# Optimization experiments

Hardware: AMD Instinct MI355X
Metric: run time of the kernel (lower is better)

Reference implementation:

```python
import jax, jax.numpy as jnp
import numpy as np


def normalize_adj(adj):
    """Symmetrize (adj + adj.T*(adj.T>adj) - adj*(adj.T>adj)), add self loops, row-normalize D^-1 A."""
    at = jnp.swapaxes(adj, -1, -2)
    mask = (at > adj).astype(adj.dtype)
    a = adj + at * mask - adj * mask
    m = a.shape[-1]
    a = a + jnp.eye(m, dtype=a.dtype)
    rowsum = a.sum(axis=-1, keepdims=True)
    inv = jnp.where(rowsum > 0, 1.0 / rowsum, 0.0)
    return a * inv


def setup_inputs() -> dict:
    key = jax.random.key(0)
    ks = jax.random.split(key, 8)
    N, n, T, dim, M = 4, 3, 512, 2048, 256
    x = jax.random.normal(ks[0], (N, n, T, dim), dtype=jnp.float32)
    nodes = jax.random.normal(ks[1], (N, M, dim), dtype=jnp.float32)
    adj = (jax.random.uniform(ks[2], (N, M, M)) < 0.05).astype(jnp.float32)
    conv_w = jax.random.normal(ks[3], (2048, dim, 3), dtype=jnp.float32) * 0.02  # OIH
    conv_b = jnp.zeros((2048,), dtype=jnp.float32)
    W1 = jax.random.normal(ks[4], (dim, dim), dtype=jnp.float32) * 0.02
    b1 = jnp.zeros((dim,), dtype=jnp.float32)
    W2 = jax.random.normal(ks[5], (dim, dim), dtype=jnp.float32) * 0.02
    b2 = jnp.zeros((dim,), dtype=jnp.float32)
    return {"x": x, "nodes": nodes, "adj": adj, "conv_w": conv_w, "conv_b": conv_b,
            "W1": W1, "b1": b1, "W2": W2, "b2": b2}


def reference(x, nodes, adj, conv_w, conv_b, W1, b1, W2, b2):
    N, n, T, dim = x.shape
    # Conv1d front-end: (N*n, C=dim, T), kernel 3, pad 1, then ReLU
    feats = x.reshape(N * n, T, dim).transpose(0, 2, 1)  # [B, C, T]
    feats = jax.lax.conv_general_dilated(
        feats, conv_w, window_strides=(1,), padding=[(1, 1)],
        dimension_numbers=("NCH", "OIH", "NCH"))
    feats = jax.nn.relu(feats + conv_b[None, :, None])
    feats = feats.transpose(0, 2, 1).reshape(N, n, T, dim)
    # GCN_Module over per-sample node graphs (batched over N)
    a = normalize_adj(adj)                                   # [N, M, M]
    h = jax.nn.relu(jnp.einsum("bij,bjf->bif", a, nodes @ W1) + b1)
    out = jnp.einsum("bij,bjf->bif", a, h @ W2) + b2         # [N, M, dim]
    return feats, out
```

## Files before the change

### kernel.cpp

```cpp
#include <hip/hip_runtime.h>
#include <stdint.h>

typedef __bf16 bf16x8 __attribute__((ext_vector_type(8)));
typedef float floatx4 __attribute__((ext_vector_type(4)));

__device__ __forceinline__ void gload_lds16(const void* g, void* l) {
    __builtin_amdgcn_global_load_lds((const __attribute__((address_space(1))) void*)g,
                                     (__attribute__((address_space(3))) void*)l, 16, 0, 0);
}

__device__ __forceinline__ uint16_t f2bf(float f) {
    uint32_t u = __float_as_uint(f);
    u += 0x7fff + ((u >> 16) & 1);
    return (uint16_t)(u >> 16);
}
__device__ __forceinline__ uint32_t f2bf2(float lo, float hi) {
    return (uint32_t)f2bf(lo) | ((uint32_t)f2bf(hi) << 16);
}

struct AmulSM {
    float vv[256];
    int   jj[256];
    float part[4];
    int   wcnt[4];
    int   woff[4];
    float sinv;
    int   n0;
};

__device__ __forceinline__ void amul_body(const float* __restrict__ adj,
                                          const float* __restrict__ H,
                                          uint16_t* __restrict__ outp,
                                          int b, int i, int tid, AmulSM* sm)
{
    const float* A = adj + ((size_t)b << 16);
    float aij = A[(i << 8) + tid];
    float aji = A[(tid << 8) + i];
    float v = fmaxf(aij, aji);
    if (tid == i) v += 1.0f;

    float s = v;
    #pragma unroll
    for (int off = 32; off > 0; off >>= 1) s += __shfl_down(s, off);

    bool pred = v != 0.0f;
    unsigned long long m = __ballot(pred);
    int wid = tid >> 6;
    if ((tid & 63) == 0) { sm->part[wid] = s; sm->wcnt[wid] = (int)__popcll(m); }
    __syncthreads();
    if (tid == 0) {
        float t = sm->part[0] + sm->part[1] + sm->part[2] + sm->part[3];
        sm->sinv = t > 0.0f ? 1.0f / t : 0.0f;
        int o = 0;
        #pragma unroll
        for (int w = 0; w < 4; ++w) { sm->woff[w] = o; o += sm->wcnt[w]; }
        sm->n0 = o;
    }
    __syncthreads();
    if (pred) {
        int pos = sm->woff[wid] + (int)__popcll(m & ((1ull << (tid & 63)) - 1ull));
        sm->vv[pos] = v * sm->sinv;
        sm->jj[pos] = tid;
    }
    __syncthreads();

    const int n0 = sm->n0;
    const int f0 = tid * 8;
    const float* Hb = H + (((size_t)b) << 8) * 2048;
    float acc[8] = {};
    for (int c = 0; c < n0; ++c) {
        float av = sm->vv[c];
        const float* hp = Hb + (size_t)sm->jj[c] * 2048 + f0;
        float4 p = *(const float4*)hp;
        float4 q = *(const float4*)(hp + 4);
        acc[0] += av * p.x; acc[1] += av * p.y; acc[2] += av * p.z; acc[3] += av * p.w;
        acc[4] += av * q.x; acc[5] += av * q.y; acc[6] += av * q.z; acc[7] += av * q.w;
    }
    uint4 o;
    o.x = f2bf2(acc[0], acc[1]);
    o.y = f2bf2(acc[2], acc[3]);
    o.z = f2bf2(acc[4], acc[5]);
    o.w = f2bf2(acc[6], acc[7]);
    *(uint4*)(outp + (((size_t)b << 8) + i) * 2048 + f0) = o;
}

#define PR_AM 1024
#define PR_W  3072
#define PR_T  5120
#define PR_N  29792

__global__ __launch_bounds__(256)
void k_prep(const float* __restrict__ x, uint32_t* __restrict__ xpad,
            const float* __restrict__ w, uint16_t* __restrict__ wT,
            const float* __restrict__ W1, const float* __restrict__ W2,
            uint16_t* __restrict__ W1T, uint16_t* __restrict__ W2T,
            const float* __restrict__ adj, const float* __restrict__ nodes,
            uint16_t* __restrict__ gbf)
{
    __shared__ union {
        float  wbuf[6144];
        float  tile[64][65];
        AmulSM am;
    } sm;
    const int bid = blockIdx.x;
    const int tid = threadIdx.x;

    if (bid < PR_AM) {
        amul_body(adj, nodes, gbf, bid >> 8, bid & 255, tid, &sm.am);
    } else if (bid < PR_W) {
        int o = bid - PR_AM;
        const float* src = w + (size_t)o * 6144;
        uint16_t*    dst = wT + (size_t)o * 6144;
        #pragma unroll
        for (int it = 0; it < 24; ++it)
            sm.wbuf[it * 256 + tid] = src[it * 256 + tid];
        __syncthreads();
        #pragma unroll
        for (int h = 0; h < 3; ++h)
            #pragma unroll
            for (int c = 0; c < 8; ++c) {
                int i = c * 256 + tid;
                dst[h * 2048 + i] = f2bf(sm.wbuf[i * 3 + h]);
            }
    } else if (bid < PR_T) {
        int t  = bid - PR_W;
        int z  = t >> 10;
        int by = (t >> 5) & 31;
        int bx = t & 31;
        const float* src = z ? W2 : W1;
        uint16_t*    dst = z ? W2T : W1T;
        int tx = tid & 63, ty = tid >> 6;
        for (int rr = ty; rr < 64; rr += 4)
            sm.tile[rr][tx] = src[(size_t)(by * 64 + rr) * 2048 + bx * 64 + tx];
        __syncthreads();
        for (int rr = ty; rr < 64; rr += 4)
            dst[(size_t)(bx * 64 + rr) * 2048 + by * 64 + tx] = f2bf(sm.tile[tx][rr]);
    } else {
        int idx2 = (bid - PR_T) * 256 + tid;
        int i2   = idx2 & 1023;
        int tmp  = idx2 >> 10;
        int b    = tmp / 514;
        int tt   = tmp - b * 514;
        float lo = 0.0f, hi = 0.0f;
        if (tt >= 1 && tt <= 512) {
            const float* s = x + ((size_t)(b * 512 + tt - 1) << 11) + i2 * 2;
            lo = s[0]; hi = s[1];
        }
        xpad[idx2] = f2bf2(lo, hi);
    }
}

__global__ __launch_bounds__(256)
void k_big(const uint16_t* __restrict__ xpad, const uint16_t* __restrict__ wmT,
           float* __restrict__ feats, const float* __restrict__ conv_b,
           const uint16_t* __restrict__ gbf, const uint16_t* __restrict__ W1T,
           float* __restrict__ h, const float* __restrict__ b1)
{
    __shared__ __align__(16) uint16_t lds[8192];
    const int bid  = blockIdx.x;
    const int tid  = threadIdx.x;
    const int lane = tid & 63;
    const int wave = tid >> 6;
    const int lm   = lane & 15;
    const int kq   = (lane >> 4) * 8;
    const int lq   = lane >> 4;
    const int srow  = tid >> 2;
    const int skcol = (tid & 3) * 8;

    if (bid < 768) {
        uint16_t* As = lds;
        uint16_t* Bs = lds + 4096;
        const int rt = (bid >> 4) * 128;
        const int ct = (bid & 15) * 128;
        const int wm = (wave >> 1) * 64;
        const int wn = (wave & 1) * 64;

        floatx4 acc[4][4] = {};

        for (int k0 = 0; k0 < 6144; k0 += 32) {
            #pragma unroll
            for (int ii = 0; ii < 2; ++ii) {
                int row = ii * 64 + srow;
                int r  = rt + row;
                int b  = r >> 9;
                int t  = r & 511;
                int kk = k0 + skcol;
                int hh = kk >> 11;
                int ic = kk & 2047;
                gload_lds16(xpad + ((size_t)(b * 514 + t + hh) << 11) + ic,
                            &As[ii * 2048 + tid * 8]);
                gload_lds16(wmT + (size_t)(ct + row) * 6144 + k0 + skcol,
                            &Bs[ii * 2048 + tid * 8]);
            }
            __syncthreads();

            bf16x8 af[4], bfr[4];
            #pragma unroll
            for (int mt = 0; mt < 4; ++mt)
                af[mt] = *(const bf16x8*)&As[(wm + mt * 16 + lm) * 32 + kq];
            #pragma unroll
            for (int nt = 0; nt < 4; ++nt)
                bfr[nt] = *(const bf16x8*)&Bs[(wn + nt * 16 + lm) * 32 + kq];
            #pragma unroll
            for (int mt = 0; mt < 4; ++mt)
                #pragma unroll
                for (int nt = 0; nt < 4; ++nt)
                    acc[mt][nt] = __builtin_amdgcn_mfma_f32_16x16x32_bf16(af[mt], bfr[nt], acc[mt][nt], 0, 0, 0);
            __syncthreads();
        }

        #pragma unroll
        for (int mt = 0; mt < 4; ++mt)
            #pragma unroll
            for (int nt = 0; nt < 4; ++nt) {
                int col = ct + wn + nt * 16 + lm;
                float bv = conv_b[col];
                #pragma unroll
                for (int r = 0; r < 4; ++r) {
                    int row = rt + wm + mt * 16 + lq * 4 + r;
                    feats[(size_t)row * 2048 + col] = fmaxf(acc[mt][nt][r] + bv, 0.0f);
                }
            }
    } else {
        uint16_t* As = lds;
        uint16_t* Bs = lds + 2048;
        const int t  = bid - 768;
        const int rt = (t >> 5) * 64;
        const int ct = (t & 31) * 64;
        const int wm = (wave >> 1) * 32;
        const int wn = (wave & 1) * 32;

        const size_t abase = (size_t)(rt + srow) * 2048 + skcol;
        const size_t bbase = (size_t)(ct + srow) * 2048 + skcol;

        floatx4 acc[2][2] = {};

        for (int k0 = 0; k0 < 2048; k0 += 32) {
            gload_lds16(gbf + abase + k0, &As[tid * 8]);
            gload_lds16(W1T + bbase + k0, &Bs[tid * 8]);
            __syncthreads();

            bf16x8 af[2], bfr[2];
            #pragma unroll
            for (int mt = 0; mt < 2; ++mt)
                af[mt] = *(const bf16x8*)&As[(wm + mt * 16 + lm) * 32 + kq];
            #pragma unroll
            for (int nt = 0; nt < 2; ++nt)
                bfr[nt] = *(const bf16x8*)&Bs[(wn + nt * 16 + lm) * 32 + kq];
            #pragma unroll
            for (int mt = 0; mt < 2; ++mt)
                #pragma unroll
                for (int nt = 0; nt < 2; ++nt)
                    acc[mt][nt] = __builtin_amdgcn_mfma_f32_16x16x32_bf16(af[mt], bfr[nt], acc[mt][nt], 0, 0, 0);
            __syncthreads();
        }

        #pragma unroll
        for (int mt = 0; mt < 2; ++mt)
            #pragma unroll
            for (int nt = 0; nt < 2; ++nt) {
                int col = ct + wn + nt * 16 + lm;
                float bv = b1[col];
                #pragma unroll
                for (int r = 0; r < 4; ++r) {
                    int row = rt + wm + mt * 16 + lq * 4 + r;
                    h[(size_t)row * 2048 + col] = fmaxf(acc[mt][nt][r] + bv, 0.0f);
                }
            }
    }
}

__global__ __launch_bounds__(256)
void k_amul(const float* __restrict__ adj, const float* __restrict__ H,
            uint16_t* __restrict__ outp)
{
    __shared__ AmulSM sm;
    amul_body(adj, H, outp, blockIdx.x >> 8, blockIdx.x & 255, threadIdx.x, &sm);
}

__global__ __launch_bounds__(256)
void k_gemm64(const uint16_t* __restrict__ A, const uint16_t* __restrict__ BT,
              float* __restrict__ C, const float* __restrict__ bias)
{
    __shared__ __align__(16) uint16_t As[64 * 32];
    __shared__ __align__(16) uint16_t Bs[64 * 32];
    const int tid  = threadIdx.x;
    const int rt   = blockIdx.y * 64;
    const int ct   = blockIdx.x * 64;
    const int lane = tid & 63;
    const int wave = tid >> 6;
    const int wm   = (wave >> 1) * 32;
    const int wn   = (wave & 1) * 32;
    const int lm   = lane & 15;
    const int kq   = (lane >> 4) * 8;
    const int srow  = tid >> 2;
    const int skcol = (tid & 3) * 8;

    const size_t abase = (size_t)(rt + srow) * 2048 + skcol;
    const size_t bbase = (size_t)(ct + srow) * 2048 + skcol;

    floatx4 acc[2][2] = {};

    for (int k0 = 0; k0 < 2048; k0 += 32) {
        gload_lds16(A  + abase + k0, &As[tid * 8]);
        gload_lds16(BT + bbase + k0, &Bs[tid * 8]);
        __syncthreads();

        bf16x8 af[2], bfr[2];
        #pragma unroll
        for (int mt = 0; mt < 2; ++mt)
            af[mt] = *(const bf16x8*)&As[(wm + mt * 16 + lm) * 32 + kq];
        #pragma unroll
        for (int nt = 0; nt < 2; ++nt)
            bfr[nt] = *(const bf16x8*)&Bs[(wn + nt * 16 + lm) * 32 + kq];
        #pragma unroll
        for (int mt = 0; mt < 2; ++mt)
            #pragma unroll
            for (int nt = 0; nt < 2; ++nt)
                acc[mt][nt] = __builtin_amdgcn_mfma_f32_16x16x32_bf16(af[mt], bfr[nt], acc[mt][nt], 0, 0, 0);
        __syncthreads();
    }

    const int lq = lane >> 4;
    #pragma unroll
    for (int mt = 0; mt < 2; ++mt)
        #pragma unroll
        for (int nt = 0; nt < 2; ++nt) {
            int col = ct + wn + nt * 16 + lm;
            float bv = bias[col];
            #pragma unroll
            for (int r = 0; r < 4; ++r) {
                int row = rt + wm + mt * 16 + lq * 4 + r;
                C[(size_t)row * 2048 + col] = acc[mt][nt][r] + bv;
            }
        }
}


extern "C" void kernel_launch(void* const* d_in, const int* in_sizes, int n_in,
                              void* d_out, int out_size, void* d_ws, size_t ws_size,
                              hipStream_t stream)
{
    const float* x      = (const float*)d_in[0];
    const float* nodes  = (const float*)d_in[1];
    const float* adj    = (const float*)d_in[2];
    const float* conv_w = (const float*)d_in[3];
    const float* conv_b = (const float*)d_in[4];
    const float* W1     = (const float*)d_in[5];
    const float* b1     = (const float*)d_in[6];
    const float* W2     = (const float*)d_in[7];
    const float* b2     = (const float*)d_in[8];
    float* out = (float*)d_out;

    char* ws = (char*)d_ws;
    uint16_t* xpad   = (uint16_t*)(ws);
    uint16_t* wmT    = (uint16_t*)(ws + 25288704);
    uint16_t* W1T    = (uint16_t*)(ws + 50454528);
    uint16_t* W2T    = (uint16_t*)(ws + 58843136);
    uint16_t* gbf    = (uint16_t*)(ws + 67231744);
    float*    h      = (float*)   (ws + 71426048);
    uint16_t* ahb    = (uint16_t*)(ws + 79814656);

    k_prep<<<PR_N, 256, 0, stream>>>(x, (uint32_t*)xpad, conv_w, wmT,
                                     W1, W2, W1T, W2T, adj, nodes, gbf);
    k_big<<<1280, 256, 0, stream>>>(xpad, wmT, out, conv_b, gbf, W1T, h, b1);
    k_amul<<<1024, 256, 0, stream>>>(adj, h, ahb);
    k_gemm64<<<dim3(32, 16), 256, 0, stream>>>(ahb, W2T, out + 12582912, b2);
}
```

Before: 427.5 us.

## Swizzle block-to-tile mapping for XCD L2 locality and move W2 transpose into k_big

Remaps block indices in the conv GEMM, the GCN GEMMs and the adjacency-multiply kernels so that blocks landing on the same XCD (bid mod 8) work on neighbouring row/column tiles, aiming to improve L2 reuse on the chiplet layout. The W2 transpose/convert work is moved from k_prep into extra trailing blocks of k_big, which shortens the prep kernel and lets that work overlap with the GEMMs. The xpad conversion now uses a float2 load. Risks include load imbalance from the tail blocks and swizzles that may not match the actual hardware dispatch order.

```diff
diff --git a/kernel.cpp b/kernel.cpp
--- a/kernel.cpp
+++ b/kernel.cpp
@@ -84,16 +84,21 @@
     *(uint4*)(outp + (((size_t)b << 8) + i) * 2048 + f0) = o;
 }
 
+__device__ __forceinline__ void amul_swizzle(int bid, int& b, int& i) {
+    int x = bid & 7, g = bid >> 3;
+    b = x >> 1;
+    i = ((x & 1) << 7) + g;
+}
+
 #define PR_AM 1024
 #define PR_W  3072
-#define PR_T  5120
-#define PR_N  29792
+#define PR_T  4096
+#define PR_N  28768
 
 __global__ __launch_bounds__(256)
 void k_prep(const float* __restrict__ x, uint32_t* __restrict__ xpad,
             const float* __restrict__ w, uint16_t* __restrict__ wT,
-            const float* __restrict__ W1, const float* __restrict__ W2,
-            uint16_t* __restrict__ W1T, uint16_t* __restrict__ W2T,
+            const float* __restrict__ W1, uint16_t* __restrict__ W1T,
             const float* __restrict__ adj, const float* __restrict__ nodes,
             uint16_t* __restrict__ gbf)
 {
@@ -106,7 +111,8 @@
     const int tid = threadIdx.x;
 
     if (bid < PR_AM) {
-        amul_body(adj, nodes, gbf, bid >> 8, bid & 255, tid, &sm.am);
+        int b, i; amul_swizzle(bid, b, i);
+        amul_body(adj, nodes, gbf, b, i, tid, &sm.am);
     } else if (bid < PR_W) {
         int o = bid - PR_AM;
         const float* src = w + (size_t)o * 6144;
@@ -124,29 +130,24 @@
             }
     } else if (bid < PR_T) {
         int t  = bid - PR_W;
-        int z  = t >> 10;
         int by = (t >> 5) & 31;
         int bx = t & 31;
-        const float* src = z ? W2 : W1;
-        uint16_t*    dst = z ? W2T : W1T;
         int tx = tid & 63, ty = tid >> 6;
         for (int rr = ty; rr < 64; rr += 4)
-            sm.tile[rr][tx] = src[(size_t)(by * 64 + rr) * 2048 + bx * 64 + tx];
+            sm.tile[rr][tx] = W1[(size_t)(by * 64 + rr) * 2048 + bx * 64 + tx];
         __syncthreads();
         for (int rr = ty; rr < 64; rr += 4)
-            dst[(size_t)(bx * 64 + rr) * 2048 + by * 64 + tx] = f2bf(sm.tile[tx][rr]);
+            W1T[(size_t)(bx * 64 + rr) * 2048 + by * 64 + tx] = f2bf(sm.tile[tx][rr]);
     } else {
         int idx2 = (bid - PR_T) * 256 + tid;
         int i2   = idx2 & 1023;
         int tmp  = idx2 >> 10;
         int b    = tmp / 514;
         int tt   = tmp - b * 514;
-        float lo = 0.0f, hi = 0.0f;
-        if (tt >= 1 && tt <= 512) {
-            const float* s = x + ((size_t)(b * 512 + tt - 1) << 11) + i2 * 2;
-            lo = s[0]; hi = s[1];
-        }
-        xpad[idx2] = f2bf2(lo, hi);
+        float2 v = {0.0f, 0.0f};
+        if (tt >= 1 && tt <= 512)
+            v = *(const float2*)(x + ((size_t)(b * 512 + tt - 1) << 11) + i2 * 2);
+        xpad[idx2] = f2bf2(v.x, v.y);
     }
 }
 
@@ -154,9 +155,13 @@
 void k_big(const uint16_t* __restrict__ xpad, const uint16_t* __restrict__ wmT,
            float* __restrict__ feats, const float* __restrict__ conv_b,
            const uint16_t* __restrict__ gbf, const uint16_t* __restrict__ W1T,
-           float* __restrict__ h, const float* __restrict__ b1)
-{
-    __shared__ __align__(16) uint16_t lds[8192];
+           float* __restrict__ h, const float* __restrict__ b1,
+           const float* __restrict__ W2, uint16_t* __restrict__ W2T)
+{
+    __shared__ __align__(16) union {
+        uint16_t u16[8192];
+        float    tile[64][65];
+    } sm;
     const int bid  = blockIdx.x;
     const int tid  = threadIdx.x;
     const int lane = tid & 63;
@@ -168,10 +173,12 @@
     const int skcol = (tid & 3) * 8;
 
     if (bid < 768) {
-        uint16_t* As = lds;
-        uint16_t* Bs = lds + 4096;
-        const int rt = (bid >> 4) * 128;
-        const int ct = (bid & 15) * 128;
+        uint16_t* As = sm.u16;
+        uint16_t* Bs = sm.u16 + 4096;
+        const int xc = bid & 7;
+        const int g  = bid >> 3;
+        const int rt = (12 * (xc >> 1) + (g % 12)) * 128;
+        const int ct = (8 * (xc & 1) + (g / 12)) * 128;
         const int wm = (wave >> 1) * 64;
         const int wn = (wave & 1) * 64;
 
@@ -221,12 +228,14 @@
                     feats[(size_t)row * 2048 + col] = fmaxf(acc[mt][nt][r] + bv, 0.0f);
                 }
             }
-    } else {
-        uint16_t* As = lds;
-        uint16_t* Bs = lds + 2048;
+    } else if (bid < 1280) {
+        uint16_t* As = sm.u16;
+        uint16_t* Bs = sm.u16 + 2048;
         const int t  = bid - 768;
-        const int rt = (t >> 5) * 64;
-        const int ct = (t & 31) * 64;
+        const int xc = t & 7;
+        const int g  = t >> 3;
+        const int rt = (g & 15) * 64;
+        const int ct = (4 * xc + (g >> 4)) * 64;
         const int wm = (wave >> 1) * 32;
         const int wn = (wave & 1) * 32;
 
@@ -267,6 +276,16 @@
                     h[(size_t)row * 2048 + col] = fmaxf(acc[mt][nt][r] + bv, 0.0f);
                 }
             }
+    } else {
+        int t  = bid - 1280;
+        int by = (t >> 5) & 31;
+        int bx = t & 31;
+        int tx = tid & 63, ty = tid >> 6;
+        for (int rr = ty; rr < 64; rr += 4)
+            sm.tile[rr][tx] = W2[(size_t)(by * 64 + rr) * 2048 + bx * 64 + tx];
+        __syncthreads();
+        for (int rr = ty; rr < 64; rr += 4)
+            W2T[(size_t)(bx * 64 + rr) * 2048 + by * 64 + tx] = f2bf(sm.tile[tx][rr]);
     }
 }
 
@@ -275,7 +294,8 @@
             uint16_t* __restrict__ outp)
 {
     __shared__ AmulSM sm;
-    amul_body(adj, H, outp, blockIdx.x >> 8, blockIdx.x & 255, threadIdx.x, &sm);
+    int b, i; amul_swizzle(blockIdx.x, b, i);
+    amul_body(adj, H, outp, b, i, threadIdx.x, &sm);
 }
 
 __global__ __launch_bounds__(256)
@@ -285,8 +305,11 @@
     __shared__ __align__(16) uint16_t As[64 * 32];
     __shared__ __align__(16) uint16_t Bs[64 * 32];
     const int tid  = threadIdx.x;
-    const int rt   = blockIdx.y * 64;
-    const int ct   = blockIdx.x * 64;
+    const int bid  = blockIdx.x;
+    const int xc   = bid & 7;
+    const int g    = bid >> 3;
+    const int rt   = (g & 15) * 64;
+    const int ct   = (4 * xc + (g >> 4)) * 64;
     const int lane = tid & 63;
     const int wave = tid >> 6;
     const int wm   = (wave >> 1) * 32;
@@ -362,8 +385,8 @@
     uint16_t* ahb    = (uint16_t*)(ws + 79814656);
 
     k_prep<<<PR_N, 256, 0, stream>>>(x, (uint32_t*)xpad, conv_w, wmT,
-                                     W1, W2, W1T, W2T, adj, nodes, gbf);
-    k_big<<<1280, 256, 0, stream>>>(xpad, wmT, out, conv_b, gbf, W1T, h, b1);
+                                     W1, W1T, adj, nodes, gbf);
+    k_big<<<2304, 256, 0, stream>>>(xpad, wmT, out, conv_b, gbf, W1T, h, b1, W2, W2T);
     k_amul<<<1024, 256, 0, stream>>>(adj, h, ahb);
-    k_gemm64<<<dim3(32, 16), 256, 0, stream>>>(ahb, W2T, out + 12582912, b2);
-}
+    k_gemm64<<<512, 256, 0, stream>>>(ahb, W2T, out + 12582912, b2);
+}
```

Measured after the change: 431.4 us. Within noise of the previous version (+0.9%).

## Double K-step per barrier, XCD-aware block swizzle, vectorize xpad conversion

Applied to the files above, without the earlier changes.

The GEMM main loops now stage two 32-wide K slices per synchronization, which halves the number of barriers and doubles the LDS footprint. Block indices are remapped so that blocks sharing A/B tiles land on the same XCD (bid&7), which should improve L2 reuse across chiplets. The xpad conversion processes four floats per thread using float4 loads, cutting the prep grid size. The duplicated 64x64 GEMM code is folded into a shared template.

```diff
diff --git a/kernel.cpp b/kernel.cpp
--- a/kernel.cpp
+++ b/kernel.cpp
@@ -84,13 +84,19 @@
     *(uint4*)(outp + (((size_t)b << 8) + i) * 2048 + f0) = o;
 }
 
+__device__ __forceinline__ void amul_swizzle(int bid, int& b, int& i) {
+    int x = bid & 7, g = bid >> 3;
+    b = x >> 1;
+    i = ((x & 1) << 7) + g;
+}
+
 #define PR_AM 1024
 #define PR_W  3072
 #define PR_T  5120
-#define PR_N  29792
+#define PR_N  17456
 
 __global__ __launch_bounds__(256)
-void k_prep(const float* __restrict__ x, uint32_t* __restrict__ xpad,
+void k_prep(const float* __restrict__ x, uint16_t* __restrict__ xpad,
             const float* __restrict__ w, uint16_t* __restrict__ wT,
             const float* __restrict__ W1, const float* __restrict__ W2,
             uint16_t* __restrict__ W1T, uint16_t* __restrict__ W2T,
@@ -106,7 +112,8 @@
     const int tid = threadIdx.x;
 
     if (bid < PR_AM) {
-        amul_body(adj, nodes, gbf, bid >> 8, bid & 255, tid, &sm.am);
+        int b, i; amul_swizzle(bid, b, i);
+        amul_body(adj, nodes, gbf, b, i, tid, &sm.am);
     } else if (bid < PR_W) {
         int o = bid - PR_AM;
         const float* src = w + (size_t)o * 6144;
@@ -136,18 +143,82 @@
         for (int rr = ty; rr < 64; rr += 4)
             dst[(size_t)(bx * 64 + rr) * 2048 + by * 64 + tx] = f2bf(sm.tile[tx][rr]);
     } else {
-        int idx2 = (bid - PR_T) * 256 + tid;
-        int i2   = idx2 & 1023;
-        int tmp  = idx2 >> 10;
+        int idx4 = (bid - PR_T) * 256 + tid;
+        int ch4  = idx4 & 511;
+        int tmp  = idx4 >> 9;
         int b    = tmp / 514;
         int tt   = tmp - b * 514;
-        float lo = 0.0f, hi = 0.0f;
-        if (tt >= 1 && tt <= 512) {
-            const float* s = x + ((size_t)(b * 512 + tt - 1) << 11) + i2 * 2;
-            lo = s[0]; hi = s[1];
-        }
-        xpad[idx2] = f2bf2(lo, hi);
-    }
+        float4 v = {0.0f, 0.0f, 0.0f, 0.0f};
+        if (tt >= 1 && tt <= 512)
+            v = *(const float4*)(x + ((size_t)(b * 512 + tt - 1) << 11) + ch4 * 4);
+        uint2 o = { f2bf2(v.x, v.y), f2bf2(v.z, v.w) };
+        ((uint2*)xpad)[idx4] = o;
+    }
+}
+
+template<bool RELU>
+__device__ __forceinline__ void g64_tile(uint16_t* As, uint16_t* Bs,
+                                         const uint16_t* __restrict__ A,
+                                         const uint16_t* __restrict__ BT,
+                                         float* __restrict__ C, const float* __restrict__ bias,
+                                         int rt, int ct)
+{
+    const int tid  = threadIdx.x;
+    const int lane = tid & 63;
+    const int wave = tid >> 6;
+    const int wm   = (wave >> 1) * 32;
+    const int wn   = (wave & 1) * 32;
+    const int lm   = lane & 15;
+    const int kq   = (lane >> 4) * 8;
+    const int sr   = tid >> 2;
+    const int sc   = (tid & 3) * 8;
+
+    const size_t abase = (size_t)(rt + sr) * 2048 + sc;
+    const size_t bbase = (size_t)(ct + sr) * 2048 + sc;
+
+    floatx4 acc[2][2] = {};
+
+    for (int k0 = 0; k0 < 2048; k0 += 64) {
+        #pragma unroll
+        for (int p = 0; p < 2; ++p) {
+            gload_lds16(A  + abase + k0 + p * 32, &As[p * 2048 + tid * 8]);
+            gload_lds16(BT + bbase + k0 + p * 32, &Bs[p * 2048 + tid * 8]);
+        }
+        __syncthreads();
+
+        #pragma unroll
+        for (int s = 0; s < 2; ++s) {
+            bf16x8 af[2], bfr[2];
+            #pragma unroll
+            for (int mt = 0; mt < 2; ++mt)
+                af[mt] = *(const bf16x8*)&As[s * 2048 + (wm + mt * 16 + lm) * 32 + kq];
+            #pragma unroll
+            for (int nt = 0; nt < 2; ++nt)
+                bfr[nt] = *(const bf16x8*)&Bs[s * 2048 + (wn + nt * 16 + lm) * 32 + kq];
+            #pragma unroll
+            for (int mt = 0; mt < 2; ++mt)
+                #pragma unroll
+                for (int nt = 0; nt < 2; ++nt)
+                    acc[mt][nt] = __builtin_amdgcn_mfma_f32_16x16x32_bf16(af[mt], bfr[nt], acc[mt][nt], 0, 0, 0);
+        }
+        __syncthreads();
+    }
+
+    const int lq = lane >> 4;
+    #pragma unroll
+    for (int mt = 0; mt < 2; ++mt)
+        #pragma unroll
+        for (int nt = 0; nt < 2; ++nt) {
+            int col = ct + wn + nt * 16 + lm;
+            float bv = bias[col];
+            #pragma unroll
+            for (int r = 0; r < 4; ++r) {
+                int row = rt + wm + mt * 16 + lq * 4 + r;
+                float v = acc[mt][nt][r] + bv;
+                if (RELU) v = fmaxf(v, 0.0f);
+                C[(size_t)row * 2048 + col] = v;
+            }
+        }
 }
 
 __global__ __launch_bounds__(256)
@@ -156,7 +227,7 @@
            const uint16_t* __restrict__ gbf, const uint16_t* __restrict__ W1T,
            float* __restrict__ h, const float* __restrict__ b1)
 {
-    __shared__ __align__(16) uint16_t lds[8192];
+    __shared__ __align__(16) uint16_t lds[16384];
     const int bid  = blockIdx.x;
     const int tid  = threadIdx.x;
     const int lane = tid & 63;
@@ -164,48 +235,60 @@
     const int lm   = lane & 15;
     const int kq   = (lane >> 4) * 8;
     const int lq   = lane >> 4;
-    const int srow  = tid >> 2;
-    const int skcol = (tid & 3) * 8;
 
     if (bid < 768) {
         uint16_t* As = lds;
-        uint16_t* Bs = lds + 4096;
-        const int rt = (bid >> 4) * 128;
-        const int ct = (bid & 15) * 128;
+        uint16_t* Bs = lds + 8192;
+        const int xc = bid & 7;
+        const int g  = bid >> 3;
+        const int rt = (12 * (xc >> 1) + (g % 12)) * 128;
+        const int ct = (8 * (xc & 1) + (g / 12)) * 128;
         const int wm = (wave >> 1) * 64;
         const int wn = (wave & 1) * 64;
 
+        const int sr = tid >> 2;
+        const int sc = (tid & 3) * 8;
+        size_t arow[2]; size_t brow[2];
+        #pragma unroll
+        for (int rh = 0; rh < 2; ++rh) {
+            int r = rt + rh * 64 + sr;
+            int b = r >> 9;
+            int t = r & 511;
+            arow[rh] = ((size_t)(b * 514 + t) << 11);
+            brow[rh] = (size_t)(ct + rh * 64 + sr) * 6144;
+        }
+
         floatx4 acc[4][4] = {};
 
-        for (int k0 = 0; k0 < 6144; k0 += 32) {
-            #pragma unroll
-            for (int ii = 0; ii < 2; ++ii) {
-                int row = ii * 64 + srow;
-                int r  = rt + row;
-                int b  = r >> 9;
-                int t  = r & 511;
-                int kk = k0 + skcol;
-                int hh = kk >> 11;
-                int ic = kk & 2047;
-                gload_lds16(xpad + ((size_t)(b * 514 + t + hh) << 11) + ic,
-                            &As[ii * 2048 + tid * 8]);
-                gload_lds16(wmT + (size_t)(ct + row) * 6144 + k0 + skcol,
-                            &Bs[ii * 2048 + tid * 8]);
+        for (int k0 = 0; k0 < 6144; k0 += 64) {
+            const int hh = k0 >> 11;
+            const int icb = (k0 & 2047) + sc;
+            #pragma unroll
+            for (int p = 0; p < 4; ++p) {
+                const int s  = p >> 1;
+                const int rh = p & 1;
+                gload_lds16(xpad + arow[rh] + ((size_t)hh << 11) + icb + s * 32,
+                            &As[p * 2048 + tid * 8]);
+                gload_lds16(wmT + brow[rh] + k0 + sc + s * 32,
+                            &Bs[p * 2048 + tid * 8]);
             }
             __syncthreads();
 
-            bf16x8 af[4], bfr[4];
-            #pragma unroll
-            for (int mt = 0; mt < 4; ++mt)
-                af[mt] = *(const bf16x8*)&As[(wm + mt * 16 + lm) * 32 + kq];
-            #pragma unroll
-            for (int nt = 0; nt < 4; ++nt)
-                bfr[nt] = *(const bf16x8*)&Bs[(wn + nt * 16 + lm) * 32 + kq];
-            #pragma unroll
-            for (int mt = 0; mt < 4; ++mt)
+            #pragma unroll
+            for (int s = 0; s < 2; ++s) {
+                bf16x8 af[4], bfr[4];
+                #pragma unroll
+                for (int mt = 0; mt < 4; ++mt)
+                    af[mt] = *(const bf16x8*)&As[s * 4096 + (wm + mt * 16 + lm) * 32 + kq];
                 #pragma unroll
                 for (int nt = 0; nt < 4; ++nt)
-                    acc[mt][nt] = __builtin_amdgcn_mfma_f32_16x16x32_bf16(af[mt], bfr[nt], acc[mt][nt], 0, 0, 0);
+                    bfr[nt] = *(const bf16x8*)&Bs[s * 4096 + (wn + nt * 16 + lm) * 32 + kq];
+                #pragma unroll
+                for (int mt = 0; mt < 4; ++mt)
+                    #pragma unroll
+                    for (int nt = 0; nt < 4; ++nt)
+                        acc[mt][nt] = __builtin_amdgcn_mfma_f32_16x16x32_bf16(af[mt], bfr[nt], acc[mt][nt], 0, 0, 0);
+            }
             __syncthreads();
         }
 
@@ -222,51 +305,12 @@
                 }
             }
     } else {
-        uint16_t* As = lds;
-        uint16_t* Bs = lds + 2048;
         const int t  = bid - 768;
-        const int rt = (t >> 5) * 64;
-        const int ct = (t & 31) * 64;
-        const int wm = (wave >> 1) * 32;
-        const int wn = (wave & 1) * 32;
-
-        const size_t abase = (size_t)(rt + srow) * 2048 + skcol;
-        const size_t bbase = (size_t)(ct + srow) * 2048 + skcol;
-
-        floatx4 acc[2][2] = {};
-
-        for (int k0 = 0; k0 < 2048; k0 += 32) {
-            gload_lds16(gbf + abase + k0, &As[tid * 8]);
-            gload_lds16(W1T + bbase + k0, &Bs[tid * 8]);
-            __syncthreads();
-
-            bf16x8 af[2], bfr[2];
-            #pragma unroll
-            for (int mt = 0; mt < 2; ++mt)
-                af[mt] = *(const bf16x8*)&As[(wm + mt * 16 + lm) * 32 + kq];
-            #pragma unroll
-            for (int nt = 0; nt < 2; ++nt)
-                bfr[nt] = *(const bf16x8*)&Bs[(wn + nt * 16 + lm) * 32 + kq];
-            #pragma unroll
-            for (int mt = 0; mt < 2; ++mt)
-                #pragma unroll
-                for (int nt = 0; nt < 2; ++nt)
-                    acc[mt][nt] = __builtin_amdgcn_mfma_f32_16x16x32_bf16(af[mt], bfr[nt], acc[mt][nt], 0, 0, 0);
-            __syncthreads();
-        }
-
-        #pragma unroll
-        for (int mt = 0; mt < 2; ++mt)
-            #pragma unroll
-            for (int nt = 0; nt < 2; ++nt) {
-                int col = ct + wn + nt * 16 + lm;
-                float bv = b1[col];
-                #pragma unroll
-                for (int r = 0; r < 4; ++r) {
-                    int row = rt + wm + mt * 16 + lq * 4 + r;
-                    h[(size_t)row * 2048 + col] = fmaxf(acc[mt][nt][r] + bv, 0.0f);
-                }
-            }
+        const int xc = t & 7;
+        const int g  = t >> 3;
+        const int rt = (g & 15) * 64;
+        const int ct = (4 * xc + (g >> 4)) * 64;
+        g64_tile<true>(lds, lds + 4096, gbf, W1T, h, b1, rt, ct);
     }
 }
 
@@ -275,65 +319,21 @@
             uint16_t* __restrict__ outp)
 {
     __shared__ AmulSM sm;
-    amul_body(adj, H, outp, blockIdx.x >> 8, blockIdx.x & 255, threadIdx.x, &sm);
+    int b, i; amul_swizzle(blockIdx.x, b, i);
+    amul_body(adj, H, outp, b, i, threadIdx.x, &sm);
 }
 
 __global__ __launch_bounds__(256)
 void k_gemm64(const uint16_t* __restrict__ A, const uint16_t* __restrict__ BT,
               float* __restrict__ C, const float* __restrict__ bias)
 {
-    __shared__ __align__(16) uint16_t As[64 * 32];
-    __shared__ __align__(16) uint16_t Bs[64 * 32];
-    const int tid  = threadIdx.x;
-    const int rt   = blockIdx.y * 64;
-    const int ct   = blockIdx.x * 64;
-    const int lane = tid & 63;
-    const int wave = tid >> 6;
-    const int wm   = (wave >> 1) * 32;
-    const int wn   = (wave & 1) * 32;
-    const int lm   = lane & 15;
-    const int kq   = (lane >> 4) * 8;
-    const int srow  = tid >> 2;
-    const int skcol = (tid & 3) * 8;
-
-    const size_t abase = (size_t)(rt + srow) * 2048 + skcol;
-    const size_t bbase = (size_t)(ct + srow) * 2048 + skcol;
-
-    floatx4 acc[2][2] = {};
-
-    for (int k0 = 0; k0 < 2048; k0 += 32) {
-        gload_lds16(A  + abase + k0, &As[tid * 8]);
-        gload_lds16(BT + bbase + k0, &Bs[tid * 8]);
-        __syncthreads();
-
-        bf16x8 af[2], bfr[2];
-        #pragma unroll
-        for (int mt = 0; mt < 2; ++mt)
-            af[mt] = *(const bf16x8*)&As[(wm + mt * 16 + lm) * 32 + kq];
-        #pragma unroll
-        for (int nt = 0; nt < 2; ++nt)
-            bfr[nt] = *(const bf16x8*)&Bs[(wn + nt * 16 + lm) * 32 + kq];
-        #pragma unroll
-        for (int mt = 0; mt < 2; ++mt)
-            #pragma unroll
-            for (int nt = 0; nt < 2; ++nt)
-                acc[mt][nt] = __builtin_amdgcn_mfma_f32_16x16x32_bf16(af[mt], bfr[nt], acc[mt][nt], 0, 0, 0);
-        __syncthreads();
-    }
-
-    const int lq = lane >> 4;
-    #pragma unroll
-    for (int mt = 0; mt < 2; ++mt)
-        #pragma unroll
-        for (int nt = 0; nt < 2; ++nt) {
-            int col = ct + wn + nt * 16 + lm;
-            float bv = bias[col];
-            #pragma unroll
-            for (int r = 0; r < 4; ++r) {
-                int row = rt + wm + mt * 16 + lq * 4 + r;
-                C[(size_t)row * 2048 + col] = acc[mt][nt][r] + bv;
-            }
-        }
+    __shared__ __align__(16) uint16_t lds[8192];
+    const int bid = blockIdx.x;
+    const int xc  = bid & 7;
+    const int g   = bid >> 3;
+    const int rt  = (g & 15) * 64;
+    const int ct  = (4 * xc + (g >> 4)) * 64;
+    g64_tile<false>(lds, lds + 4096, A, BT, C, bias, rt, ct);
 }
 
 
@@ -361,9 +361,9 @@
     float*    h      = (float*)   (ws + 71426048);
     uint16_t* ahb    = (uint16_t*)(ws + 79814656);
 
-    k_prep<<<PR_N, 256, 0, stream>>>(x, (uint32_t*)xpad, conv_w, wmT,
+    k_prep<<<PR_N, 256, 0, stream>>>(x, xpad, conv_w, wmT,
                                      W1, W2, W1T, W2T, adj, nodes, gbf);
     k_big<<<1280, 256, 0, stream>>>(xpad, wmT, out, conv_b, gbf, W1T, h, b1);
     k_amul<<<1024, 256, 0, stream>>>(adj, h, ahb);
-    k_gemm64<<<dim3(32, 16), 256, 0, stream>>>(ahb, W2T, out + 12582912, b2);
-}
+    k_gemm64<<<512, 256, 0, stream>>>(ahb, W2T, out + 12582912, b2);
+}
```

Result: faster. 411.9 us (-3.6%).
